# Kernel optimization log

Hardware: AMD Instinct MI355X
Metric: run time of the kernel (lower is better)

## Reference

```python
import jax, jax.numpy as jnp
import numpy as np

N = 40000      # nodes
E = 20000      # hyperedges
M = 640000     # incidences
D = 128        # num_features == num_classes == MLP_hidden
ALPHA = 0.1
EPS = 1e-5


def _layernorm(h, g, b):
    mu = jnp.mean(h, axis=-1, keepdims=True)
    var = jnp.mean((h - mu) ** 2, axis=-1, keepdims=True)
    return (h - mu) * jax.lax.rsqrt(var + EPS) * g + b


def _mlp(x, w1, b1, g, be, w2, b2):
    h = x @ w1 + b1
    h = jax.nn.relu(_layernorm(h, g, be))
    return h @ w2 + b2


def _scatter_mean(vals, idx, num_segments):
    s = jax.ops.segment_sum(vals, idx, num_segments=num_segments)
    cnt = jax.ops.segment_sum(jnp.ones((vals.shape[0],), vals.dtype), idx,
                              num_segments=num_segments)
    return s / jnp.maximum(cnt, 1.0)[:, None]


def setup_inputs() -> dict:
    key = jax.random.key(0)
    ks = jax.random.split(key, 16)
    x = jax.random.normal(ks[0], (N, D), dtype=jnp.float32)
    vertex = jax.random.randint(ks[1], (M,), 0, N)
    edges = jax.random.randint(ks[2], (M,), 0, E)
    edge_index = jnp.stack([vertex, edges]).astype(jnp.int64)

    def lin(k, fin, fout):
        s = 1.0 / np.sqrt(fin)
        kw, kb = jax.random.split(k)
        return (jax.random.uniform(kw, (fin, fout), jnp.float32, -s, s),
                jax.random.uniform(kb, (fout,), jnp.float32, -s, s))

    w1_1, b1_1 = lin(ks[3], D, D)
    w1_2, b1_2 = lin(ks[4], D, D)
    w2_1, b2_1 = lin(ks[5], 2 * D, D)
    w2_2, b2_2 = lin(ks[6], D, D)
    g1 = jnp.ones((D,), jnp.float32)
    be1 = jnp.zeros((D,), jnp.float32)
    g2 = jnp.ones((D,), jnp.float32)
    be2 = jnp.zeros((D,), jnp.float32)
    return {"x": x, "w1_1": w1_1, "b1_1": b1_1, "g1": g1, "be1": be1,
            "w1_2": w1_2, "b1_2": b1_2, "w2_1": w2_1, "b2_1": b2_1,
            "g2": g2, "be2": be2, "w2_2": w2_2, "b2_2": b2_2,
            "edge_index": edge_index}


def reference(x, w1_1, b1_1, g1, be1, w1_2, b1_2,
              w2_1, b2_1, g2, be2, w2_2, b2_2, edge_index):
    vertex = edge_index[0]
    edges = edge_index[1]
    X0 = x
    # gather -> MLP1 -> scatter-mean onto hyperedges
    Xve = _mlp(x[vertex], w1_1, b1_1, g1, be1, w1_2, b1_2)   # [M, D]
    Xe = _scatter_mean(Xve, edges, E)                         # [E, D]
    # gather back -> concat -> MLP2 -> scatter-mean onto nodes
    Xev = Xe[edges]                                           # [M, D]
    Xev = _mlp(jnp.concatenate([x[vertex], Xev], axis=-1),
               w2_1, b2_1, g2, be2, w2_2, b2_2)               # [M, D]
    Xv = _scatter_mean(Xev, vertex, N)                        # [N, D]
    return (1.0 - ALPHA) * Xv + ALPHA * X0
```

## Files before the change

### kernel.cpp

```cpp
#include <hip/hip_runtime.h>

#define DF 128
constexpr int NN = 40000;
constexpr int EE = 20000;
constexpr int MM = 640000;
constexpr float EPSF = 1e-5f;
constexpr float ALPHA = 0.1f;
constexpr int SE = 96;
constexpr int SV = 64;

constexpr int NB_G1 = (NN + 63) / 64;
constexpr int NB_G2 = (NN + 63) / 64;
constexpr int NB_GEMMS = NB_G1 + NB_G2;
constexpr int NB_BUILD = 5000;

__device__ __forceinline__ int cidxE(int e) { return (e & 7) * (EE >> 3) + (e >> 3); }
__device__ __forceinline__ int cidxV(int v) { return (v & 7) * (NN >> 3) + (v >> 3); }

__global__ __launch_bounds__(256) void prek(int* __restrict__ cnt,
                                            const float* __restrict__ w1_2,
                                            const float* __restrict__ b1_2,
                                            const float* __restrict__ w2_1,
                                            float* __restrict__ Wc,
                                            float* __restrict__ bc) {
  int b = blockIdx.x;
  if (b < 235) {
    int i = b * 256 + threadIdx.x;
    if (i < 60000) cnt[i] = 0;
  } else {
    const float* w2b = w2_1 + 128 * DF;
    int out = (b - 235) * 256 + threadIdx.x;
    if (out < 16384) {
      int i = out >> 7;
      int j = out & 127;
      float s = 0.0f;
      for (int k = 0; k < 128; ++k) s += w1_2[i * DF + k] * w2b[k * DF + j];
      Wc[out] = s;
    } else if (out < 16512) {
      int j = out - 16384;
      float s = 0.0f;
      for (int k = 0; k < 128; ++k) s += b1_2[k] * w2b[k * DF + j];
      bc[j] = s;
    }
  }
}

template <int EPI, bool STATS>
__device__ __forceinline__ void gemm_tile(const float* __restrict__ A, int nrows,
                                          const float* __restrict__ W,
                                          const float* __restrict__ bias,
                                          const int* __restrict__ cnt,
                                          const float* __restrict__ xres,
                                          float* __restrict__ C,
                                          float* __restrict__ sOut,
                                          float* __restrict__ qOut,
                                          int blk, float* as) {
  int tid = threadIdx.x;
  int rbase = blk * 64;

  #pragma unroll
  for (int j = 0; j < 8; ++j) {
    int q = tid + j * 256;
    int row = q >> 5;
    int c4 = q & 31;
    int grow = rbase + row;
    float4 v = make_float4(0.f, 0.f, 0.f, 0.f);
    if (grow < nrows) {
      v = *reinterpret_cast<const float4*>(A + (size_t)grow * DF + c4 * 4);
    }
    *reinterpret_cast<float4*>(&as[row * 132 + c4 * 4]) = v;
  }
  __syncthreads();

  int tc = tid & 15;
  int tr = tid >> 4;
  int cbase = tc * 8;

  float acc[4][8];
  #pragma unroll
  for (int i = 0; i < 4; ++i)
    #pragma unroll
    for (int c = 0; c < 8; ++c) acc[i][c] = 0.0f;

  #pragma unroll 4
  for (int k = 0; k < 128; ++k) {
    float w[8];
    *reinterpret_cast<float4*>(&w[0]) = *reinterpret_cast<const float4*>(W + k * DF + cbase);
    *reinterpret_cast<float4*>(&w[4]) = *reinterpret_cast<const float4*>(W + k * DF + cbase + 4);
    float a[4];
    #pragma unroll
    for (int i = 0; i < 4; ++i) a[i] = as[(tr * 4 + i) * 132 + k];
    #pragma unroll
    for (int i = 0; i < 4; ++i)
      #pragma unroll
      for (int c = 0; c < 8; ++c) acc[i][c] += a[i] * w[c];
  }

  if (bias) {
    #pragma unroll
    for (int i = 0; i < 4; ++i)
      #pragma unroll
      for (int c = 0; c < 8; ++c) acc[i][c] += bias[cbase + c];
  }

  if (STATS) {
    #pragma unroll
    for (int i = 0; i < 4; ++i) {
      float s = 0.f, q = 0.f;
      #pragma unroll
      for (int c = 0; c < 8; ++c) { s += acc[i][c]; q += acc[i][c] * acc[i][c]; }
      #pragma unroll
      for (int mask = 1; mask <= 8; mask <<= 1) {
        s += __shfl_xor(s, mask, 16);
        q += __shfl_xor(q, mask, 16);
      }
      if (tc == 0) {
        int grow = rbase + tr * 4 + i;
        if (grow < nrows) { sOut[grow] = s; qOut[grow] = q; }
      }
    }
  }

  #pragma unroll
  for (int i = 0; i < 4; ++i) {
    int grow = rbase + tr * 4 + i;
    if (grow >= nrows) continue;
    float outv[8];
    if (EPI == 2) {
      int cv = cnt[(grow & 7) * (NN >> 3) + (grow >> 3)];
      #pragma unroll
      for (int c = 0; c < 8; ++c) {
        float xv = xres[(size_t)grow * DF + cbase + c];
        outv[c] = (cv == 0) ? ALPHA * xv : (1.0f - ALPHA) * acc[i][c] + ALPHA * xv;
      }
    } else {
      #pragma unroll
      for (int c = 0; c < 8; ++c) outv[c] = acc[i][c];
    }
    *reinterpret_cast<float4*>(C + (size_t)grow * DF + cbase) =
        make_float4(outv[0], outv[1], outv[2], outv[3]);
    *reinterpret_cast<float4*>(C + (size_t)grow * DF + cbase + 4) =
        make_float4(outv[4], outv[5], outv[6], outv[7]);
  }
}

__device__ __forceinline__ void gemm_tile_double(const float* __restrict__ x,
                                                 const float* __restrict__ W1,
                                                 const float* __restrict__ b1,
                                                 const float* __restrict__ g,
                                                 const float* __restrict__ be,
                                                 const float* __restrict__ W2,
                                                 float* __restrict__ G,
                                                 int blk, float* as) {
  int tid = threadIdx.x;
  int rbase = blk * 64;

  #pragma unroll
  for (int j = 0; j < 8; ++j) {
    int q = tid + j * 256;
    int row = q >> 5;
    int c4 = q & 31;
    int grow = rbase + row;
    float4 v = make_float4(0.f, 0.f, 0.f, 0.f);
    if (grow < NN) {
      v = *reinterpret_cast<const float4*>(x + (size_t)grow * DF + c4 * 4);
    }
    *reinterpret_cast<float4*>(&as[row * 132 + c4 * 4]) = v;
  }
  __syncthreads();

  int tc = tid & 15;
  int tr = tid >> 4;
  int cbase = tc * 8;

  float acc[4][8];
  #pragma unroll
  for (int i = 0; i < 4; ++i)
    #pragma unroll
    for (int c = 0; c < 8; ++c) acc[i][c] = 0.0f;

  #pragma unroll 4
  for (int k = 0; k < 128; ++k) {
    float w[8];
    *reinterpret_cast<float4*>(&w[0]) = *reinterpret_cast<const float4*>(W1 + k * DF + cbase);
    *reinterpret_cast<float4*>(&w[4]) = *reinterpret_cast<const float4*>(W1 + k * DF + cbase + 4);
    float a[4];
    #pragma unroll
    for (int i = 0; i < 4; ++i) a[i] = as[(tr * 4 + i) * 132 + k];
    #pragma unroll
    for (int i = 0; i < 4; ++i)
      #pragma unroll
      for (int c = 0; c < 8; ++c) acc[i][c] += a[i] * w[c];
  }

  float gv[8], bev[8];
  #pragma unroll
  for (int c = 0; c < 8; ++c) { gv[c] = g[cbase + c]; bev[c] = be[cbase + c]; }
  #pragma unroll
  for (int i = 0; i < 4; ++i) {
    #pragma unroll
    for (int c = 0; c < 8; ++c) acc[i][c] += b1[cbase + c];
    float s = 0.f, s2 = 0.f;
    #pragma unroll
    for (int c = 0; c < 8; ++c) { s += acc[i][c]; s2 += acc[i][c] * acc[i][c]; }
    #pragma unroll
    for (int mask = 1; mask <= 8; mask <<= 1) {
      s += __shfl_xor(s, mask, 16);
      s2 += __shfl_xor(s2, mask, 16);
    }
    float mean = s * (1.0f / 128.0f);
    float var = s2 * (1.0f / 128.0f) - mean * mean;
    float rs = rsqrtf(var + EPSF);
    #pragma unroll
    for (int c = 0; c < 8; ++c) {
      float y = (acc[i][c] - mean) * rs * gv[c] + bev[c];
      acc[i][c] = fmaxf(y, 0.0f);
    }
  }

  __syncthreads();
  #pragma unroll
  for (int i = 0; i < 4; ++i)
    #pragma unroll
    for (int c = 0; c < 8; ++c) as[(tr * 4 + i) * 132 + cbase + c] = acc[i][c];
  __syncthreads();

  #pragma unroll
  for (int i = 0; i < 4; ++i)
    #pragma unroll
    for (int c = 0; c < 8; ++c) acc[i][c] = 0.0f;

  #pragma unroll 4
  for (int k = 0; k < 128; ++k) {
    float w[8];
    *reinterpret_cast<float4*>(&w[0]) = *reinterpret_cast<const float4*>(W2 + k * DF + cbase);
    *reinterpret_cast<float4*>(&w[4]) = *reinterpret_cast<const float4*>(W2 + k * DF + cbase + 4);
    float a[4];
    #pragma unroll
    for (int i = 0; i < 4; ++i) a[i] = as[(tr * 4 + i) * 132 + k];
    #pragma unroll
    for (int i = 0; i < 4; ++i)
      #pragma unroll
      for (int c = 0; c < 8; ++c) acc[i][c] += a[i] * w[c];
  }

  #pragma unroll
  for (int i = 0; i < 4; ++i) {
    int grow = rbase + tr * 4 + i;
    if (grow >= NN) continue;
    *reinterpret_cast<float4*>(G + (size_t)grow * DF + cbase) =
        make_float4(acc[i][0], acc[i][1], acc[i][2], acc[i][3]);
    *reinterpret_cast<float4*>(G + (size_t)grow * DF + cbase + 4) =
        make_float4(acc[i][4], acc[i][5], acc[i][6], acc[i][7]);
  }
}

__global__ __launch_bounds__(256) void fusedA(
    const int* __restrict__ ei,
    int* __restrict__ cnt_e, int* __restrict__ cnt_v,
    ushort* __restrict__ lst_e, ushort* __restrict__ lst_v,
    const float* __restrict__ x,
    const float* __restrict__ w1_1, const float* __restrict__ b1_1,
    const float* __restrict__ g1, const float* __restrict__ be1,
    const float* __restrict__ w2_1, const float* __restrict__ Wc,
    float* __restrict__ G, float* __restrict__ A2,
    float* __restrict__ sA, float* __restrict__ qA) {
  __shared__ float as[64 * 132];
  int blk = blockIdx.x;
  if (blk < NB_G1) {
    gemm_tile_double(x, w1_1, b1_1, g1, be1, Wc, G, blk, as);
  } else if (blk < NB_GEMMS) {
    gemm_tile<0, true>(x, NN, w2_1, nullptr, nullptr, nullptr, A2, sA, qA,
                       blk - NB_G1, as);
  } else {
    int b = blk - NB_GEMMS;
    int role = blk & 7;
    int group = b >> 3;
    #pragma unroll
    for (int k = 0; k < 4; ++k) {
      int m = (group * 4 + k) * 256 + threadIdx.x;
      int v = ei[m];
      int e = ei[MM + m];
      if ((e & 7) == role) {
        int pe = atomicAdd(&cnt_e[role * (EE >> 3) + (e >> 3)], 1);
        lst_e[e * SE + pe] = (ushort)v;
      }
      if ((v & 7) == role) {
        int pv = atomicAdd(&cnt_v[role * (NN >> 3) + (v >> 3)], 1);
        lst_v[v * SV + pv] = (ushort)e;
      }
    }
  }
}

template <int EPI, bool STATS>
__global__ __launch_bounds__(256) void gemm128(const float* __restrict__ A, int nrows,
                                               const float* __restrict__ W,
                                               const float* __restrict__ bias,
                                               const int* __restrict__ cnt,
                                               const float* __restrict__ xres,
                                               float* __restrict__ C,
                                               float* __restrict__ sOut,
                                               float* __restrict__ qOut) {
  __shared__ float as[64 * 132];
  gemm_tile<EPI, STATS>(A, nrows, W, bias, cnt, xres, C, sOut, qOut,
                        blockIdx.x, as);
}

__global__ __launch_bounds__(256) void gather1B(const float* __restrict__ G,
                                                const int* __restrict__ cnt_e,
                                                const ushort* __restrict__ lst_e,
                                                const float* __restrict__ bcv,
                                                const float* __restrict__ b21,
                                                float* __restrict__ B,
                                                float* __restrict__ sB,
                                                float* __restrict__ qB) {
  int e = blockIdx.x * 4 + (threadIdx.x >> 6);
  int lane = threadIdx.x & 63;
  int g = lane >> 4;
  int l = lane & 15;
  int deg = cnt_e[cidxE(e)];
  const ushort* lst = lst_e + e * SE;
  float4 acc0 = make_float4(0.f, 0.f, 0.f, 0.f);
  float4 acc1 = make_float4(0.f, 0.f, 0.f, 0.f);
  for (int i = g; i < deg; i += 4) {
    int v = lst[i];
    const float* src = G + (size_t)v * DF + l * 8;
    float4 h0 = *reinterpret_cast<const float4*>(src);
    float4 h1 = *reinterpret_cast<const float4*>(src + 4);
    acc0.x += h0.x; acc0.y += h0.y; acc0.z += h0.z; acc0.w += h0.w;
    acc1.x += h1.x; acc1.y += h1.y; acc1.z += h1.z; acc1.w += h1.w;
  }
  #pragma unroll
  for (int mask = 16; mask <= 32; mask <<= 1) {
    acc0.x += __shfl_xor(acc0.x, mask); acc0.y += __shfl_xor(acc0.y, mask);
    acc0.z += __shfl_xor(acc0.z, mask); acc0.w += __shfl_xor(acc0.w, mask);
    acc1.x += __shfl_xor(acc1.x, mask); acc1.y += __shfl_xor(acc1.y, mask);
    acc1.z += __shfl_xor(acc1.z, mask); acc1.w += __shfl_xor(acc1.w, mask);
  }
  if (g == 0) {
    float sc = 1.0f / (float)(deg > 1 ? deg : 1);
    float b[8];
    b[0] = acc0.x * sc + bcv[l * 8 + 0] + b21[l * 8 + 0];
    b[1] = acc0.y * sc + bcv[l * 8 + 1] + b21[l * 8 + 1];
    b[2] = acc0.z * sc + bcv[l * 8 + 2] + b21[l * 8 + 2];
    b[3] = acc0.w * sc + bcv[l * 8 + 3] + b21[l * 8 + 3];
    b[4] = acc1.x * sc + bcv[l * 8 + 4] + b21[l * 8 + 4];
    b[5] = acc1.y * sc + bcv[l * 8 + 5] + b21[l * 8 + 5];
    b[6] = acc1.z * sc + bcv[l * 8 + 6] + b21[l * 8 + 6];
    b[7] = acc1.w * sc + bcv[l * 8 + 7] + b21[l * 8 + 7];
    float* dst = B + (size_t)e * DF + l * 8;
    *reinterpret_cast<float4*>(dst) = make_float4(b[0], b[1], b[2], b[3]);
    *reinterpret_cast<float4*>(dst + 4) = make_float4(b[4], b[5], b[6], b[7]);
    float s = 0.f, q = 0.f;
    #pragma unroll
    for (int j = 0; j < 8; ++j) { s += b[j]; q += b[j] * b[j]; }
    #pragma unroll
    for (int mask = 1; mask <= 8; mask <<= 1) {
      s += __shfl_xor(s, mask, 16);
      q += __shfl_xor(q, mask, 16);
    }
    if (l == 0) { sB[e] = s; qB[e] = q; }
  }
}

__global__ __launch_bounds__(256) void gather2(const float* __restrict__ A2,
                                               const float* __restrict__ B,
                                               const float* __restrict__ sA,
                                               const float* __restrict__ qA,
                                               const float* __restrict__ sB,
                                               const float* __restrict__ qB,
                                               const int* __restrict__ cnt_v,
                                               const ushort* __restrict__ lst_v,
                                               const float* __restrict__ g2,
                                               const float* __restrict__ be2,
                                               float* __restrict__ Svmean) {
  int v = blockIdx.x * 4 + (threadIdx.x >> 6);
  int lane = threadIdx.x & 63;
  int g = lane >> 4;
  int l = lane & 15;
  const float* ap = A2 + (size_t)v * DF + l * 8;
  float4 a0 = *reinterpret_cast<const float4*>(ap);
  float4 a1 = *reinterpret_cast<const float4*>(ap + 4);
  float4 gv0 = *reinterpret_cast<const float4*>(g2 + l * 8);
  float4 gv1 = *reinterpret_cast<const float4*>(g2 + l * 8 + 4);
  float4 bv0 = *reinterpret_cast<const float4*>(be2 + l * 8);
  float4 bv1 = *reinterpret_cast<const float4*>(be2 + l * 8 + 4);
  float sAv = sA[v];
  float qAv = qA[v];
  int deg = cnt_v[cidxV(v)];
  const ushort* lst = lst_v + v * SV;
  float4 acc0 = make_float4(0.f, 0.f, 0.f, 0.f);
  float4 acc1 = make_float4(0.f, 0.f, 0.f, 0.f);
  for (int i = g; i < deg; i += 4) {
    int e = lst[i];
    const float* bp = B + (size_t)e * DF + l * 8;
    float4 b0 = *reinterpret_cast<const float4*>(bp);
    float4 b1 = *reinterpret_cast<const float4*>(bp + 4);
    float d = a0.x * b0.x + a0.y * b0.y + a0.z * b0.z + a0.w * b0.w +
              a1.x * b1.x + a1.y * b1.y + a1.z * b1.z + a1.w * b1.w;
    d += __shfl_xor(d, 1, 16);
    d += __shfl_xor(d, 2, 16);
    d += __shfl_xor(d, 4, 16);
    d += __shfl_xor(d, 8, 16);
    float s = sAv + sB[e];
    float q = qAv + qB[e] + 2.0f * d;
    float mean = s * (1.0f / 128.0f);
    float var = q * (1.0f / 128.0f) - mean * mean;
    float rs = rsqrtf(var + EPSF);
    float mrs = mean * rs;
    float t;
    t = (a0.x + b0.x) * rs - mrs; acc0.x += fmaxf(t * gv0.x + bv0.x, 0.f);
    t = (a0.y + b0.y) * rs - mrs; acc0.y += fmaxf(t * gv0.y + bv0.y, 0.f);
    t = (a0.z + b0.z) * rs - mrs; acc0.z += fmaxf(t * gv0.z + bv0.z, 0.f);
    t = (a0.w + b0.w) * rs - mrs; acc0.w += fmaxf(t * gv0.w + bv0.w, 0.f);
    t = (a1.x + b1.x) * rs - mrs; acc1.x += fmaxf(t * gv1.x + bv1.x, 0.f);
    t = (a1.y + b1.y) * rs - mrs; acc1.y += fmaxf(t * gv1.y + bv1.y, 0.f);
    t = (a1.z + b1.z) * rs - mrs; acc1.z += fmaxf(t * gv1.z + bv1.z, 0.f);
    t = (a1.w + b1.w) * rs - mrs; acc1.w += fmaxf(t * gv1.w + bv1.w, 0.f);
  }
  #pragma unroll
  for (int mask = 16; mask <= 32; mask <<= 1) {
    acc0.x += __shfl_xor(acc0.x, mask); acc0.y += __shfl_xor(acc0.y, mask);
    acc0.z += __shfl_xor(acc0.z, mask); acc0.w += __shfl_xor(acc0.w, mask);
    acc1.x += __shfl_xor(acc1.x, mask); acc1.y += __shfl_xor(acc1.y, mask);
    acc1.z += __shfl_xor(acc1.z, mask); acc1.w += __shfl_xor(acc1.w, mask);
  }
  if (g == 0) {
    float sc = 1.0f / (float)(deg > 1 ? deg : 1);
    float* dst = Svmean + (size_t)v * DF + l * 8;
    *reinterpret_cast<float4*>(dst) =
        make_float4(acc0.x * sc, acc0.y * sc, acc0.z * sc, acc0.w * sc);
    *reinterpret_cast<float4*>(dst + 4) =
        make_float4(acc1.x * sc, acc1.y * sc, acc1.z * sc, acc1.w * sc);
  }
}

extern "C" void kernel_launch(void* const* d_in, const int* in_sizes, int n_in,
                              void* d_out, int out_size, void* d_ws, size_t ws_size,
                              hipStream_t stream) {
  const float* x    = (const float*)d_in[0];
  const float* w1_1 = (const float*)d_in[1];
  const float* b1_1 = (const float*)d_in[2];
  const float* g1   = (const float*)d_in[3];
  const float* be1  = (const float*)d_in[4];
  const float* w1_2 = (const float*)d_in[5];
  const float* b1_2 = (const float*)d_in[6];
  const float* w2_1 = (const float*)d_in[7];
  const float* b2_1 = (const float*)d_in[8];
  const float* g2   = (const float*)d_in[9];
  const float* be2  = (const float*)d_in[10];
  const float* w2_2 = (const float*)d_in[11];
  const float* b2_2 = (const float*)d_in[12];
  const int* ei     = (const int*)d_in[13];
  float* out = (float*)d_out;

  float* ws = (float*)d_ws;
  float* bufN1 = ws;
  float* bufN2 = ws + 5120000;
  float* bufE  = ws + 10240000;
  float* Wc    = ws + 12800000;
  float* bc    = ws + 12816384;
  float* sA    = ws + 12816512;
  float* qA    = ws + 12856512;
  float* sB    = ws + 12896512;
  float* qB    = ws + 12916512;
  int*   ints  = (int*)(ws + 12936512);
  int* cnt_e  = ints;
  int* cnt_v  = ints + 20000;
  ushort* lst_e = (ushort*)(ints + 60000);
  ushort* lst_v = (ushort*)(ints + 60000 + 960000);

  prek<<<300, 256, 0, stream>>>(cnt_e, w1_2, b1_2, w2_1, Wc, bc);

  fusedA<<<NB_GEMMS + NB_BUILD, 256, 0, stream>>>(
      ei, cnt_e, cnt_v, lst_e, lst_v, x, w1_1, b1_1, g1, be1, w2_1, Wc,
      bufN1, bufN2, sA, qA);

  gather1B<<<EE / 4, 256, 0, stream>>>(bufN1, cnt_e, lst_e, bc, b2_1,
                                       bufE, sB, qB);

  gather2<<<NN / 4, 256, 0, stream>>>(bufN2, bufE, sA, qA, sB, qB,
                                      cnt_v, lst_v, g2, be2, bufN1);

  gemm128<2, false><<<(NN + 63) / 64, 256, 0, stream>>>(
      bufN1, NN, w2_2, b2_2, cnt_v, x, out, nullptr, nullptr);
}
```

Measured before the change: 327.1 us.

## Move vertex-list build into gather1 kernel and use nontemporal stores/loads

Splits the incidence-list construction so only the hyperedge lists are built alongside the first GEMMs. The vertex lists are now built in a new fused kernel that also runs the hyperedge gather, which spreads the atomic build work across two launches and overlaps it with different compute. It also switches the GEMM output stores and the edge-index loads to nontemporal builtins to reduce cache pollution. The edge index is now read twice, and nontemporal stores of G and C may hurt if those buffers are re-read soon afterwards.

```diff
diff --git a/kernel.cpp b/kernel.cpp
--- a/kernel.cpp
+++ b/kernel.cpp
@@ -12,10 +12,18 @@
 constexpr int NB_G1 = (NN + 63) / 64;
 constexpr int NB_G2 = (NN + 63) / 64;
 constexpr int NB_GEMMS = NB_G1 + NB_G2;
-constexpr int NB_BUILD = 5000;
+constexpr int NB_EBUILD = 5000;
+constexpr int NB_GB1 = EE / 4;
+constexpr int NB_VBUILD = 5000;
 
 __device__ __forceinline__ int cidxE(int e) { return (e & 7) * (EE >> 3) + (e >> 3); }
 __device__ __forceinline__ int cidxV(int v) { return (v & 7) * (NN >> 3) + (v >> 3); }
+
+typedef float f32x4 __attribute__((ext_vector_type(4)));
+__device__ __forceinline__ void nt_store4(float* p, float a, float b, float c, float d) {
+  f32x4 v = {a, b, c, d};
+  __builtin_nontemporal_store(v, (f32x4*)p);
+}
 
 __global__ __launch_bounds__(256) void prek(int* __restrict__ cnt,
                                             const float* __restrict__ w1_2,
@@ -137,10 +145,8 @@
       #pragma unroll
       for (int c = 0; c < 8; ++c) outv[c] = acc[i][c];
     }
-    *reinterpret_cast<float4*>(C + (size_t)grow * DF + cbase) =
-        make_float4(outv[0], outv[1], outv[2], outv[3]);
-    *reinterpret_cast<float4*>(C + (size_t)grow * DF + cbase + 4) =
-        make_float4(outv[4], outv[5], outv[6], outv[7]);
+    nt_store4(C + (size_t)grow * DF + cbase, outv[0], outv[1], outv[2], outv[3]);
+    nt_store4(C + (size_t)grow * DF + cbase + 4, outv[4], outv[5], outv[6], outv[7]);
   }
 }
 
@@ -248,17 +254,14 @@
   for (int i = 0; i < 4; ++i) {
     int grow = rbase + tr * 4 + i;
     if (grow >= NN) continue;
-    *reinterpret_cast<float4*>(G + (size_t)grow * DF + cbase) =
-        make_float4(acc[i][0], acc[i][1], acc[i][2], acc[i][3]);
-    *reinterpret_cast<float4*>(G + (size_t)grow * DF + cbase + 4) =
-        make_float4(acc[i][4], acc[i][5], acc[i][6], acc[i][7]);
+    nt_store4(G + (size_t)grow * DF + cbase, acc[i][0], acc[i][1], acc[i][2], acc[i][3]);
+    nt_store4(G + (size_t)grow * DF + cbase + 4, acc[i][4], acc[i][5], acc[i][6], acc[i][7]);
   }
 }
 
 __global__ __launch_bounds__(256) void fusedA(
     const int* __restrict__ ei,
-    int* __restrict__ cnt_e, int* __restrict__ cnt_v,
-    ushort* __restrict__ lst_e, ushort* __restrict__ lst_v,
+    int* __restrict__ cnt_e, ushort* __restrict__ lst_e,
     const float* __restrict__ x,
     const float* __restrict__ w1_1, const float* __restrict__ b1_1,
     const float* __restrict__ g1, const float* __restrict__ be1,
@@ -279,12 +282,81 @@
     #pragma unroll
     for (int k = 0; k < 4; ++k) {
       int m = (group * 4 + k) * 256 + threadIdx.x;
-      int v = ei[m];
-      int e = ei[MM + m];
+      int v = __builtin_nontemporal_load(ei + m);
+      int e = __builtin_nontemporal_load(ei + MM + m);
       if ((e & 7) == role) {
         int pe = atomicAdd(&cnt_e[role * (EE >> 3) + (e >> 3)], 1);
         lst_e[e * SE + pe] = (ushort)v;
       }
+    }
+  }
+}
+
+__global__ __launch_bounds__(256) void fusedB(
+    const float* __restrict__ G,
+    const int* __restrict__ cnt_e, const ushort* __restrict__ lst_e,
+    const float* __restrict__ bcv, const float* __restrict__ b21,
+    float* __restrict__ B, float* __restrict__ sB, float* __restrict__ qB,
+    const int* __restrict__ ei,
+    int* __restrict__ cnt_v, ushort* __restrict__ lst_v) {
+  int blk = blockIdx.x;
+  if (blk < NB_GB1) {
+    int e = blk * 4 + (threadIdx.x >> 6);
+    int lane = threadIdx.x & 63;
+    int g = lane >> 4;
+    int l = lane & 15;
+    int deg = cnt_e[cidxE(e)];
+    const ushort* lst = lst_e + e * SE;
+    float4 acc0 = make_float4(0.f, 0.f, 0.f, 0.f);
+    float4 acc1 = make_float4(0.f, 0.f, 0.f, 0.f);
+    for (int i = g; i < deg; i += 4) {
+      int v = lst[i];
+      const float* src = G + (size_t)v * DF + l * 8;
+      float4 h0 = *reinterpret_cast<const float4*>(src);
+      float4 h1 = *reinterpret_cast<const float4*>(src + 4);
+      acc0.x += h0.x; acc0.y += h0.y; acc0.z += h0.z; acc0.w += h0.w;
+      acc1.x += h1.x; acc1.y += h1.y; acc1.z += h1.z; acc1.w += h1.w;
+    }
+    #pragma unroll
+    for (int mask = 16; mask <= 32; mask <<= 1) {
+      acc0.x += __shfl_xor(acc0.x, mask); acc0.y += __shfl_xor(acc0.y, mask);
+      acc0.z += __shfl_xor(acc0.z, mask); acc0.w += __shfl_xor(acc0.w, mask);
+      acc1.x += __shfl_xor(acc1.x, mask); acc1.y += __shfl_xor(acc1.y, mask);
+      acc1.z += __shfl_xor(acc1.z, mask); acc1.w += __shfl_xor(acc1.w, mask);
+    }
+    if (g == 0) {
+      float sc = 1.0f / (float)(deg > 1 ? deg : 1);
+      float b[8];
+      b[0] = acc0.x * sc + bcv[l * 8 + 0] + b21[l * 8 + 0];
+      b[1] = acc0.y * sc + bcv[l * 8 + 1] + b21[l * 8 + 1];
+      b[2] = acc0.z * sc + bcv[l * 8 + 2] + b21[l * 8 + 2];
+      b[3] = acc0.w * sc + bcv[l * 8 + 3] + b21[l * 8 + 3];
+      b[4] = acc1.x * sc + bcv[l * 8 + 4] + b21[l * 8 + 4];
+      b[5] = acc1.y * sc + bcv[l * 8 + 5] + b21[l * 8 + 5];
+      b[6] = acc1.z * sc + bcv[l * 8 + 6] + b21[l * 8 + 6];
+      b[7] = acc1.w * sc + bcv[l * 8 + 7] + b21[l * 8 + 7];
+      float* dst = B + (size_t)e * DF + l * 8;
+      *reinterpret_cast<float4*>(dst) = make_float4(b[0], b[1], b[2], b[3]);
+      *reinterpret_cast<float4*>(dst + 4) = make_float4(b[4], b[5], b[6], b[7]);
+      float s = 0.f, q = 0.f;
+      #pragma unroll
+      for (int j = 0; j < 8; ++j) { s += b[j]; q += b[j] * b[j]; }
+      #pragma unroll
+      for (int mask = 1; mask <= 8; mask <<= 1) {
+        s += __shfl_xor(s, mask, 16);
+        q += __shfl_xor(q, mask, 16);
+      }
+      if (l == 0) { sB[e] = s; qB[e] = q; }
+    }
+  } else {
+    int b = blk - NB_GB1;
+    int role = blk & 7;
+    int group = b >> 3;
+    #pragma unroll
+    for (int k = 0; k < 4; ++k) {
+      int m = (group * 4 + k) * 256 + threadIdx.x;
+      int v = __builtin_nontemporal_load(ei + m);
+      int e = __builtin_nontemporal_load(ei + MM + m);
       if ((v & 7) == role) {
         int pv = atomicAdd(&cnt_v[role * (NN >> 3) + (v >> 3)], 1);
         lst_v[v * SV + pv] = (ushort)e;
@@ -305,63 +377,6 @@
   __shared__ float as[64 * 132];
   gemm_tile<EPI, STATS>(A, nrows, W, bias, cnt, xres, C, sOut, qOut,
                         blockIdx.x, as);
-}
-
-__global__ __launch_bounds__(256) void gather1B(const float* __restrict__ G,
-                                                const int* __restrict__ cnt_e,
-                                                const ushort* __restrict__ lst_e,
-                                                const float* __restrict__ bcv,
-                                                const float* __restrict__ b21,
-                                                float* __restrict__ B,
-                                                float* __restrict__ sB,
-                                                float* __restrict__ qB) {
-  int e = blockIdx.x * 4 + (threadIdx.x >> 6);
-  int lane = threadIdx.x & 63;
-  int g = lane >> 4;
-  int l = lane & 15;
-  int deg = cnt_e[cidxE(e)];
-  const ushort* lst = lst_e + e * SE;
-  float4 acc0 = make_float4(0.f, 0.f, 0.f, 0.f);
-  float4 acc1 = make_float4(0.f, 0.f, 0.f, 0.f);
-  for (int i = g; i < deg; i += 4) {
-    int v = lst[i];
-    const float* src = G + (size_t)v * DF + l * 8;
-    float4 h0 = *reinterpret_cast<const float4*>(src);
-    float4 h1 = *reinterpret_cast<const float4*>(src + 4);
-    acc0.x += h0.x; acc0.y += h0.y; acc0.z += h0.z; acc0.w += h0.w;
-    acc1.x += h1.x; acc1.y += h1.y; acc1.z += h1.z; acc1.w += h1.w;
-  }
-  #pragma unroll
-  for (int mask = 16; mask <= 32; mask <<= 1) {
-    acc0.x += __shfl_xor(acc0.x, mask); acc0.y += __shfl_xor(acc0.y, mask);
-    acc0.z += __shfl_xor(acc0.z, mask); acc0.w += __shfl_xor(acc0.w, mask);
-    acc1.x += __shfl_xor(acc1.x, mask); acc1.y += __shfl_xor(acc1.y, mask);
-    acc1.z += __shfl_xor(acc1.z, mask); acc1.w += __shfl_xor(acc1.w, mask);
-  }
-  if (g == 0) {
-    float sc = 1.0f / (float)(deg > 1 ? deg : 1);
-    float b[8];
-    b[0] = acc0.x * sc + bcv[l * 8 + 0] + b21[l * 8 + 0];
-    b[1] = acc0.y * sc + bcv[l * 8 + 1] + b21[l * 8 + 1];
-    b[2] = acc0.z * sc + bcv[l * 8 + 2] + b21[l * 8 + 2];
-    b[3] = acc0.w * sc + bcv[l * 8 + 3] + b21[l * 8 + 3];
-    b[4] = acc1.x * sc + bcv[l * 8 + 4] + b21[l * 8 + 4];
-    b[5] = acc1.y * sc + bcv[l * 8 + 5] + b21[l * 8 + 5];
-    b[6] = acc1.z * sc + bcv[l * 8 + 6] + b21[l * 8 + 6];
-    b[7] = acc1.w * sc + bcv[l * 8 + 7] + b21[l * 8 + 7];
-    float* dst = B + (size_t)e * DF + l * 8;
-    *reinterpret_cast<float4*>(dst) = make_float4(b[0], b[1], b[2], b[3]);
-    *reinterpret_cast<float4*>(dst + 4) = make_float4(b[4], b[5], b[6], b[7]);
-    float s = 0.f, q = 0.f;
-    #pragma unroll
-    for (int j = 0; j < 8; ++j) { s += b[j]; q += b[j] * b[j]; }
-    #pragma unroll
-    for (int mask = 1; mask <= 8; mask <<= 1) {
-      s += __shfl_xor(s, mask, 16);
-      q += __shfl_xor(q, mask, 16);
-    }
-    if (l == 0) { sB[e] = s; qB[e] = q; }
-  }
 }
 
 __global__ __launch_bounds__(256) void gather2(const float* __restrict__ A2,
@@ -473,12 +488,12 @@
 
   prek<<<300, 256, 0, stream>>>(cnt_e, w1_2, b1_2, w2_1, Wc, bc);
 
-  fusedA<<<NB_GEMMS + NB_BUILD, 256, 0, stream>>>(
-      ei, cnt_e, cnt_v, lst_e, lst_v, x, w1_1, b1_1, g1, be1, w2_1, Wc,
+  fusedA<<<NB_GEMMS + NB_EBUILD, 256, 0, stream>>>(
+      ei, cnt_e, lst_e, x, w1_1, b1_1, g1, be1, w2_1, Wc,
       bufN1, bufN2, sA, qA);
 
-  gather1B<<<EE / 4, 256, 0, stream>>>(bufN1, cnt_e, lst_e, bc, b2_1,
-                                       bufE, sB, qB);
+  fusedB<<<NB_GB1 + NB_VBUILD, 256, 0, stream>>>(
+      bufN1, cnt_e, lst_e, bc, b2_1, bufE, sB, qB, ei, cnt_v, lst_v);
 
   gather2<<<NN / 4, 256, 0, stream>>>(bufN2, bufE, sA, qA, sB, qB,
                                       cnt_v, lst_v, g2, be2, bufN1);
```

Result: slower. 347.6 us (+6.3%).
